# Kernel optimization log

Measured on AMD Instinct MI355X. Metric: run time of the kernel, lower is better.

## Reference

```python
import jax, jax.numpy as jnp
import numpy as np
import math

B, D, E = 32768, 256, 8          # batch, feature dim (shape=[256]), num_steps experts
T_TOTAL = 1.0
H_STEP = T_TOTAL / E             # self.h
EIGMIN, EIGINIT, EIGMAX = -1.0, 0.0, 1.0
LOGIT_099 = math.log(0.99 / 0.01)


def setup_inputs() -> dict:
    key = jax.random.key(0)
    k_t, k_y, k_w1, k_w2 = jax.random.split(key, 4)
    std = 1.0 / math.sqrt(D)     # xavier-ish init for expert weights
    return {
        "t": jax.random.uniform(k_t, (B,), dtype=jnp.float32),            # times in [0, T)
        "y": jax.random.normal(k_y, (B, D), dtype=jnp.float32),
        "W1": jax.random.normal(k_w1, (E, D, D), dtype=jnp.float32) * std,
        "b1": jnp.zeros((E, D), dtype=jnp.float32),
        "W2": jax.random.normal(k_w2, (E, D, D), dtype=jnp.float32) * std,
        "b2": jnp.zeros((E, D), dtype=jnp.float32),
        "scales": jnp.full((1, D), LOGIT_099, dtype=jnp.float32),         # learn_scales=False init
        "shifta": jnp.asarray(LOGIT_099, dtype=jnp.float32),
        "shiftb": jnp.asarray(LOGIT_099, dtype=jnp.float32),
    }


def reference(t, y, W1, b1, W2, b2, scales, shifta, shiftb):
    # t2ind: clamp(int(t / h), max=E-1)
    ind = jnp.minimum((t / H_STEP).astype(jnp.int32), E - 1)            # [B]
    # per-sample dispatch to expert F[i] (2-layer MLP), grouped as masked
    # dense batched GEMMs per expert (E is a small fixed set)
    f = jnp.zeros_like(y)
    for e in range(E):
        h_e = jnp.tanh(jnp.einsum('bd,kd->bk', y, W1[e]) + b1[e])       # [B, D]
        f_e = jnp.einsum('bd,kd->bk', h_e, W2[e]) + b2[e]               # [B, D]
        f = jnp.where((ind == e)[:, None], f_e, f)
    # sigmoid-scale / affine-combine epilogue
    f = jax.nn.sigmoid(scales) * f
    a = EIGINIT + jax.nn.sigmoid(shifta) * (EIGMIN - EIGINIT)
    b = EIGINIT + jax.nn.sigmoid(shiftb) * (EIGMAX - EIGINIT)
    return 0.5 * ((b - a) * f + (a + b) * y)
```

## Files before the change

kernel.cpp:

```cpp
#include <hip/hip_runtime.h>

#define BATCH 32768
#define DIM   256
#define NEXP  8
#define MT    32
#define STRIDE 264

typedef __bf16 bf16x8 __attribute__((ext_vector_type(8)));
typedef __bf16 bf16x4 __attribute__((ext_vector_type(4)));
typedef float  f32x16 __attribute__((ext_vector_type(16)));

static __device__ __forceinline__ float sigmoid_f(float x) {
    return __builtin_amdgcn_rcpf(1.f + __expf(-x));
}
static __device__ __forceinline__ float tanh_f(float x) {
    return 1.f - 2.f * __builtin_amdgcn_rcpf(__expf(2.f * x) + 1.f);
}

__global__ void prep_kernel(const float* __restrict__ W1, const float* __restrict__ W2,
                            const float* __restrict__ t,
                            bf16x8* __restrict__ W1p, bf16x8* __restrict__ W2p,
                            int* __restrict__ cursor, int* __restrict__ idxb) {
    const int b = blockIdx.x;
    if (b < 256) {
        const int tid = b * 256 + threadIdx.x;
        const int kh  = tid & 1;
        const int ks  = (tid >> 1) & 15;
        const int col = (tid >> 5) & 255;
        const int e   = tid >> 13;
        const long src = (long)tid * 8;
        const float4 a0 = *(const float4*)(W1 + src);
        const float4 a1 = *(const float4*)(W1 + src + 4);
        const float4 c0 = *(const float4*)(W2 + src);
        const float4 c1 = *(const float4*)(W2 + src + 4);
        bf16x8 w1, w2;
        w1[0] = (__bf16)a0.x; w1[1] = (__bf16)a0.y; w1[2] = (__bf16)a0.z; w1[3] = (__bf16)a0.w;
        w1[4] = (__bf16)a1.x; w1[5] = (__bf16)a1.y; w1[6] = (__bf16)a1.z; w1[7] = (__bf16)a1.w;
        w2[0] = (__bf16)c0.x; w2[1] = (__bf16)c0.y; w2[2] = (__bf16)c0.z; w2[3] = (__bf16)c0.w;
        w2[4] = (__bf16)c1.x; w2[5] = (__bf16)c1.y; w2[6] = (__bf16)c1.z; w2[7] = (__bf16)c1.w;
        const int dst = (e << 13) | ((col >> 5) << 10) | (ks << 6) | (kh << 5) | (col & 31);
        W1p[dst] = w1;
        W2p[dst] = w2;
    } else {
        __shared__ int h[NEXP], base[NEXP];
        if (threadIdx.x < NEXP) h[threadIdx.x] = 0;
        __syncthreads();
        const int i = (b - 256) * 256 + threadIdx.x;
        const int e = min((int)(t[i] * 8.0f), NEXP - 1);
        const int lr = atomicAdd(&h[e], 1);
        __syncthreads();
        if (threadIdx.x < NEXP)
            base[threadIdx.x] = atomicAdd(&cursor[threadIdx.x], h[threadIdx.x]);
        __syncthreads();
        idxb[e * BATCH + base[e] + lr] = i;
    }
}

__global__ void __launch_bounds__(512, 8)
mlp_kernel(const float* __restrict__ y,
           const float* __restrict__ scales,
           const float* __restrict__ shifta,
           const float* __restrict__ shiftb,
           const float* __restrict__ b1,
           const float* __restrict__ b2,
           const bf16x8* __restrict__ W1p,
           const bf16x8* __restrict__ W2p,
           const int* __restrict__ cnt,
           const int* __restrict__ idxb,
           float* __restrict__ out) {
    __shared__ __bf16 ab[MT * STRIDE];
    __shared__ int rows[MT];

    const int tx   = threadIdx.x;
    const int wave = tx >> 6;
    const int lane = tx & 63;
    const int nl   = lane & 31;
    const int kh   = lane >> 5;
    const int ncol = wave * 32;

    int c[NEXP], tp[NEXP + 1];
    tp[0] = 0;
#pragma unroll
    for (int e = 0; e < NEXP; ++e) {
        c[e] = cnt[e];
        tp[e + 1] = tp[e] + ((c[e] + MT - 1) >> 5);
    }
    const int total = tp[NEXP];

    const float sa = sigmoid_f(shifta[0]);
    const float sb = sigmoid_f(shiftb[0]);
    const float av = -sa;
    const float bvv = sb;
    const float k1 = 0.5f * (bvv - av);
    const float k2 = 0.5f * (av + bvv);
    const bool needy = (k2 != 0.0f);

    for (int tile = blockIdx.x; tile < total; tile += gridDim.x) {
        int e = 0;
#pragma unroll
        for (int j = 0; j < NEXP; ++j) if (tile >= tp[j + 1]) e = j + 1;
        const int rbase = (tile - tp[e]) * MT;
        const int nrows = min(MT, c[e] - rbase);
        const int* idx_e = idxb + e * BATCH;

        __syncthreads();
#pragma unroll
        for (int pass = 0; pass < 4; ++pass) {
            const int r  = pass * 8 + wave;
            const int rr = min(r, nrows - 1);
            const int g  = idx_e[rbase + rr];
            if (lane == 0) rows[r] = (r < nrows) ? g : -1;
            const float4 v = *(const float4*)(y + (long)g * DIM + lane * 4);
            bf16x4 w;
            w[0] = (__bf16)v.x; w[1] = (__bf16)v.y; w[2] = (__bf16)v.z; w[3] = (__bf16)v.w;
            *(bf16x4*)(ab + r * STRIDE + lane * 4) = w;
        }
        __syncthreads();

        const __bf16* apt0 = ab + nl * STRIDE + kh * 8;

        const bf16x8* w1p = W1p + (e << 13) + (wave << 10) + lane;
        f32x16 acc = {};
#pragma unroll
        for (int ks = 0; ks < 16; ++ks) {
            bf16x8 a0 = *(const bf16x8*)(apt0 + ks * 16);
            bf16x8 bb = w1p[ks << 6];
            acc = __builtin_amdgcn_mfma_f32_32x32x16_bf16(a0, bb, acc, 0, 0, 0);
        }
        __syncthreads();

        {
            const int n = ncol + nl;
            const float b1v = b1[(e << 8) | n];
#pragma unroll
            for (int r = 0; r < 16; ++r) {
                const int row = (r & 3) + ((r >> 2) << 3) + (kh << 2);
                ab[row * STRIDE + n] = (__bf16)tanh_f(acc[r] + b1v);
            }
        }
        __syncthreads();

        const bf16x8* w2p = W2p + (e << 13) + (wave << 10) + lane;
        f32x16 acc2 = {};
#pragma unroll
        for (int ks = 0; ks < 16; ++ks) {
            bf16x8 a0 = *(const bf16x8*)(apt0 + ks * 16);
            bf16x8 bb = w2p[ks << 6];
            acc2 = __builtin_amdgcn_mfma_f32_32x32x16_bf16(a0, bb, acc2, 0, 0, 0);
        }

        {
            const int n = ncol + nl;
            const float c1  = k1 * sigmoid_f(scales[n]);
            const float b2v = b2[(e << 8) | n];
#pragma unroll
            for (int r = 0; r < 16; ++r) {
                const int row = (r & 3) + ((r >> 2) << 3) + (kh << 2);
                const int g = rows[row];
                if (g >= 0) {
                    float res = c1 * (acc2[r] + b2v);
                    if (needy) res += k2 * y[(long)g * DIM + n];
                    out[(long)g * DIM + n] = res;
                }
            }
        }
    }
}

extern "C" void kernel_launch(void* const* d_in, const int* in_sizes, int n_in,
                              void* d_out, int out_size, void* d_ws, size_t ws_size,
                              hipStream_t stream) {
    const float* t      = (const float*)d_in[0];
    const float* y      = (const float*)d_in[1];
    const float* W1     = (const float*)d_in[2];
    const float* b1     = (const float*)d_in[3];
    const float* W2     = (const float*)d_in[4];
    const float* b2     = (const float*)d_in[5];
    const float* scales = (const float*)d_in[6];
    const float* shifta = (const float*)d_in[7];
    const float* shiftb = (const float*)d_in[8];
    float* out = (float*)d_out;

    char* ws = (char*)d_ws;
    int* cursor = (int*)ws;
    int* idxb   = (int*)(ws + 256);
    bf16x8* W1p = (bf16x8*)(ws + 256 + NEXP * BATCH * 4);
    bf16x8* W2p = W1p + 65536;

    hipMemsetAsync(cursor, 0, 32, stream);
    prep_kernel<<<384, 256, 0, stream>>>(W1, W2, t, W1p, W2p, cursor, idxb);
    mlp_kernel<<<1032, 512, 0, stream>>>(y, scales, shifta, shiftb, b1, b2,
                                         W1p, W2p, cursor, idxb, out);
}
```

Before: 133.3 us.

## Pin expert weights in registers per block and prefetch next tile's rows

Switches to a persistent grid of 256 blocks: 8 experts with 32 blocks each. Each block loads its expert's W1/W2 fragments into registers once, instead of reloading them from global memory for every tile. The next tile's gathered y rows are loaded into registers while the current tile's MFMAs run, overlapping gather latency with compute. This costs much higher register pressure (launch bounds lowered to 2 blocks per CU). Load balance now depends on how many tokens each expert gets, since a block handles only one expert.

New measurement: 124.8 us. -6.4%, faster.

```diff
diff --git a/kernel.cpp b/kernel.cpp
--- a/kernel.cpp
+++ b/kernel.cpp
@@ -56,7 +56,7 @@
     }
 }
 
-__global__ void __launch_bounds__(512, 8)
+__global__ void __launch_bounds__(512, 2)
 mlp_kernel(const float* __restrict__ y,
            const float* __restrict__ scales,
            const float* __restrict__ shifta,
@@ -76,37 +76,40 @@
     const int lane = tx & 63;
     const int nl   = lane & 31;
     const int kh   = lane >> 5;
-    const int ncol = wave * 32;
-
-    int c[NEXP], tp[NEXP + 1];
-    tp[0] = 0;
-#pragma unroll
-    for (int e = 0; e < NEXP; ++e) {
-        c[e] = cnt[e];
-        tp[e + 1] = tp[e] + ((c[e] + MT - 1) >> 5);
-    }
-    const int total = tp[NEXP];
+    const int n    = wave * 32 + nl;
+
+    const int e    = blockIdx.x >> 5;
+    const int slot = blockIdx.x & 31;
+    const int ce   = cnt[e];
+    const int nt_e = (ce + MT - 1) >> 5;
+    if (slot >= nt_e) return;
+    const int* idx_e = idxb + e * BATCH;
+
+    const bf16x8* w1p = W1p + (e << 13) + (wave << 10) + lane;
+    const bf16x8* w2p = W2p + (e << 13) + (wave << 10) + lane;
+    bf16x8 wA[16], wB[16];
+#pragma unroll
+    for (int ks = 0; ks < 16; ++ks) {
+        wA[ks] = w1p[ks << 6];
+        wB[ks] = w2p[ks << 6];
+    }
 
     const float sa = sigmoid_f(shifta[0]);
     const float sb = sigmoid_f(shiftb[0]);
-    const float av = -sa;
-    const float bvv = sb;
-    const float k1 = 0.5f * (bvv - av);
-    const float k2 = 0.5f * (av + bvv);
+    const float k1 = 0.5f * (sb + sa);
+    const float k2 = 0.5f * (sb - sa);
     const bool needy = (k2 != 0.0f);
-
-    for (int tile = blockIdx.x; tile < total; tile += gridDim.x) {
-        int e = 0;
-#pragma unroll
-        for (int j = 0; j < NEXP; ++j) if (tile >= tp[j + 1]) e = j + 1;
-        const int rbase = (tile - tp[e]) * MT;
-        const int nrows = min(MT, c[e] - rbase);
-        const int* idx_e = idxb + e * BATCH;
-
-        __syncthreads();
-#pragma unroll
-        for (int pass = 0; pass < 4; ++pass) {
-            const int r  = pass * 8 + wave;
+    const float c1  = k1 * sigmoid_f(scales[n]);
+    const float b1v = b1[(e << 8) | n];
+    const float b2v = b2[(e << 8) | n];
+
+    int ti = slot;
+    int nrows = min(MT, ce - ti * MT);
+    {
+        const int rbase = ti * MT;
+#pragma unroll
+        for (int p = 0; p < 4; ++p) {
+            const int r  = p * 8 + wave;
             const int rr = min(r, nrows - 1);
             const int g  = idx_e[rbase + rr];
             if (lane == 0) rows[r] = (r < nrows) ? g : -1;
@@ -115,55 +118,80 @@
             w[0] = (__bf16)v.x; w[1] = (__bf16)v.y; w[2] = (__bf16)v.z; w[3] = (__bf16)v.w;
             *(bf16x4*)(ab + r * STRIDE + lane * 4) = w;
         }
-        __syncthreads();
+    }
+    __syncthreads();
+
+    for (;;) {
+        const int ti2 = ti + 32;
+        const bool have_next = (ti2 < nt_e);
+        int nrows2 = 0;
+        int g2v[4];
+        float4 v2[4];
+        if (have_next) {
+            nrows2 = min(MT, ce - ti2 * MT);
+            const int rbase2 = ti2 * MT;
+#pragma unroll
+            for (int p = 0; p < 4; ++p) {
+                const int r  = p * 8 + wave;
+                const int rr = min(r, nrows2 - 1);
+                g2v[p] = idx_e[rbase2 + rr];
+            }
+#pragma unroll
+            for (int p = 0; p < 4; ++p)
+                v2[p] = *(const float4*)(y + (long)g2v[p] * DIM + lane * 4);
+        }
 
         const __bf16* apt0 = ab + nl * STRIDE + kh * 8;
 
-        const bf16x8* w1p = W1p + (e << 13) + (wave << 10) + lane;
         f32x16 acc = {};
 #pragma unroll
         for (int ks = 0; ks < 16; ++ks) {
             bf16x8 a0 = *(const bf16x8*)(apt0 + ks * 16);
-            bf16x8 bb = w1p[ks << 6];
-            acc = __builtin_amdgcn_mfma_f32_32x32x16_bf16(a0, bb, acc, 0, 0, 0);
-        }
-        __syncthreads();
-
-        {
-            const int n = ncol + nl;
-            const float b1v = b1[(e << 8) | n];
-#pragma unroll
-            for (int r = 0; r < 16; ++r) {
-                const int row = (r & 3) + ((r >> 2) << 3) + (kh << 2);
-                ab[row * STRIDE + n] = (__bf16)tanh_f(acc[r] + b1v);
-            }
-        }
-        __syncthreads();
-
-        const bf16x8* w2p = W2p + (e << 13) + (wave << 10) + lane;
+            acc = __builtin_amdgcn_mfma_f32_32x32x16_bf16(a0, wA[ks], acc, 0, 0, 0);
+        }
+        __syncthreads();
+
+#pragma unroll
+        for (int r = 0; r < 16; ++r) {
+            const int row = (r & 3) + ((r >> 2) << 3) + (kh << 2);
+            ab[row * STRIDE + n] = (__bf16)tanh_f(acc[r] + b1v);
+        }
+        __syncthreads();
+
         f32x16 acc2 = {};
 #pragma unroll
         for (int ks = 0; ks < 16; ++ks) {
             bf16x8 a0 = *(const bf16x8*)(apt0 + ks * 16);
-            bf16x8 bb = w2p[ks << 6];
-            acc2 = __builtin_amdgcn_mfma_f32_32x32x16_bf16(a0, bb, acc2, 0, 0, 0);
-        }
-
-        {
-            const int n = ncol + nl;
-            const float c1  = k1 * sigmoid_f(scales[n]);
-            const float b2v = b2[(e << 8) | n];
-#pragma unroll
-            for (int r = 0; r < 16; ++r) {
-                const int row = (r & 3) + ((r >> 2) << 3) + (kh << 2);
-                const int g = rows[row];
-                if (g >= 0) {
-                    float res = c1 * (acc2[r] + b2v);
-                    if (needy) res += k2 * y[(long)g * DIM + n];
-                    out[(long)g * DIM + n] = res;
-                }
+            acc2 = __builtin_amdgcn_mfma_f32_32x32x16_bf16(a0, wB[ks], acc2, 0, 0, 0);
+        }
+
+#pragma unroll
+        for (int r = 0; r < 16; ++r) {
+            const int row = (r & 3) + ((r >> 2) << 3) + (kh << 2);
+            const int g = rows[row];
+            if (g >= 0) {
+                float res = c1 * (acc2[r] + b2v);
+                if (needy) res += k2 * y[(long)g * DIM + n];
+                out[(long)g * DIM + n] = res;
             }
         }
+
+        if (!have_next) return;
+
+        __syncthreads();
+
+#pragma unroll
+        for (int p = 0; p < 4; ++p) {
+            const int r = p * 8 + wave;
+            if (lane == 0) rows[r] = (r < nrows2) ? g2v[p] : -1;
+            const float4 v = v2[p];
+            bf16x4 w;
+            w[0] = (__bf16)v.x; w[1] = (__bf16)v.y; w[2] = (__bf16)v.z; w[3] = (__bf16)v.w;
+            *(bf16x4*)(ab + r * STRIDE + lane * 4) = w;
+        }
+        __syncthreads();
+
+        ti = ti2; nrows = nrows2;
     }
 }
 
@@ -189,6 +217,6 @@
 
     hipMemsetAsync(cursor, 0, 32, stream);
     prep_kernel<<<384, 256, 0, stream>>>(W1, W2, t, W1p, W2p, cursor, idxb);
-    mlp_kernel<<<1032, 512, 0, stream>>>(y, scales, shifta, shiftb, b1, b2,
-                                         W1p, W2p, cursor, idxb, out);
-}
+    mlp_kernel<<<256, 512, 0, stream>>>(y, scales, shifta, shiftb, b1, b2,
+                                        W1p, W2p, cursor, idxb, out);
+}
```
